# Kernel tuning notes

Hardware: AMD Instinct MI355X
Metric: run time of the kernel (lower is better)

## Reference

```python
import jax, jax.numpy as jnp
import numpy as np

# irreps = 128x0e + 64x1o + 32x2e  ->  dim = 128 + 192 + 160 = 480
IRREPS = [(128, 0), (64, 1), (32, 2)]  # (multiplicity, l)
NUM_SCALAR = 128          # 0e channels (p=+1, l=0); scalar_index = [0..127]
NUM_FEATURES = 224        # total irrep instances
DIM = 480
EPS_LN = 1e-5             # unused by math path (kept for fidelity to signature)
EPS_INV = 1e-6            # Invariant eps (default)
N = 100000


def setup_inputs() -> dict:
    key = jax.random.key(0)
    k1, k2, k3 = jax.random.split(key, 3)
    node_input = jax.random.normal(k1, (N, DIM), dtype=jnp.float32)
    affine_weight = jax.random.normal(k2, (NUM_FEATURES,), dtype=jnp.float32)
    affine_bias = jax.random.normal(k3, (NUM_SCALAR,), dtype=jnp.float32)
    return {"node_input": node_input, "affine_weight": affine_weight, "affine_bias": affine_bias}


def _eln(x, weight, bias):
    # 1) subtract mean of scalar (0e) channels from those channels only
    scalar_mean = jnp.mean(x[:, :NUM_SCALAR], axis=1, keepdims=True)
    x = x.at[:, :NUM_SCALAR].add(-scalar_mean)

    # 2) per-irrep-instance norm: Invariant = Norm(x + eps^2) - eps
    norms = []
    off = 0
    for mul, l in IRREPS:
        d = 2 * l + 1
        blk = x[:, off: off + mul * d].reshape(x.shape[0], mul, d)
        n = jnp.sqrt(jnp.sum(jnp.square(blk + EPS_INV ** 2), axis=-1)) - EPS_INV
        norms.append(n)
        off += mul * d
    norm = jnp.concatenate(norms, axis=1)  # [N, num_features]

    # 3) RMS over irrep instances, scale whole feature vector
    inv_rms = jax.lax.rsqrt(jnp.mean(jnp.square(norm), axis=1, keepdims=True))
    x = x * inv_rms

    # 4) per-irrep affine scale (ElementwiseTensorProduct with num_features x 0e)
    w_parts = []
    ix = 0
    for mul, l in IRREPS:
        d = 2 * l + 1
        w_parts.append(jnp.repeat(weight[ix: ix + mul], d))
        ix += mul
    w_full = jnp.concatenate(w_parts)  # [dim]
    x = x * w_full[None, :]

    # 5) add bias to scalar channels
    x = x.at[:, :NUM_SCALAR].add(bias[None, :])
    return x


def reference(node_input, affine_weight, affine_bias):
    return _eln(node_input, affine_weight, affine_bias)
```

## Files before the change

### kernel.cpp

```cpp
#include <hip/hip_runtime.h>
#include <hip/hip_bf16.h>


#define DIM 480

typedef float f32x4 __attribute__((ext_vector_type(4)));

__global__ __launch_bounds__(256) void eln_kernel(
    const float* __restrict__ in,
    const float* __restrict__ wgt,
    const float* __restrict__ bias,
    float* __restrict__ out,
    int n_rows)
{
    const int lane    = threadIdx.x & 63;
    const int gwave   = (blockIdx.x * blockDim.x + threadIdx.x) >> 6;
    const int n_waves = (gridDim.x * blockDim.x) >> 6;

    float w0k[4], w1k[4], bk[4];
    #pragma unroll
    for (int k = 0; k < 4; ++k) {
        int j = 4 * lane + k;
        if (j < 128) { w0k[k] = wgt[j];                       bk[k] = bias[j]; }
        else         { w0k[k] = wgt[128 + (j - 128) / 3];     bk[k] = 0.f;     }
    }
    #pragma unroll
    for (int k = 0; k < 4; ++k) {
        if (lane < 56) {
            int j = 256 + 4 * lane + k;
            w1k[k] = (j < 320) ? wgt[128 + (j - 128) / 3]
                               : wgt[192 + (j - 320) / 5];
        } else {
            w1k[k] = 0.f;
        }
    }

    const float epsq = 1e-12f;

    for (int row = gwave; row < n_rows; row += n_waves) {
        const f32x4* xr = reinterpret_cast<const f32x4*>(in + (size_t)row * DIM);
        f32x4*       yr = reinterpret_cast<f32x4*>(out + (size_t)row * DIM);

        f32x4 r0 = __builtin_nontemporal_load(xr + lane);
        f32x4 r1 = (f32x4)(0.f);
        if (lane < 56) r1 = __builtin_nontemporal_load(xr + 64 + lane);

        float ssum = (lane < 32) ? (r0.x + r0.y + r0.z + r0.w) : 0.f;
        #pragma unroll
        for (int m = 1; m < 64; m <<= 1) ssum += __shfl_xor(ssum, m);
        const float mean = ssum * (1.0f / 128.0f);
        if (lane < 32) { r0.x -= mean; r0.y -= mean; r0.z -= mean; r0.w -= mean; }

        float a0 = r0.x + epsq, a1 = r0.y + epsq, a2 = r0.z + epsq, a3 = r0.w + epsq;
        float nsq = a0 * a0 + a1 * a1 + a2 * a2 + a3 * a3;
        if (lane < 56) {
            float c0 = r1.x + epsq, c1 = r1.y + epsq, c2 = r1.z + epsq, c3 = r1.w + epsq;
            nsq += c0 * c0 + c1 * c1 + c2 * c2 + c3 * c3;
        }
        #pragma unroll
        for (int m = 1; m < 64; m <<= 1) nsq += __shfl_xor(nsq, m);
        const float inv_rms = rsqrtf(nsq * (1.0f / 224.0f));

        f32x4 o0;
        o0.x = r0.x * inv_rms * w0k[0] + bk[0];
        o0.y = r0.y * inv_rms * w0k[1] + bk[1];
        o0.z = r0.z * inv_rms * w0k[2] + bk[2];
        o0.w = r0.w * inv_rms * w0k[3] + bk[3];
        __builtin_nontemporal_store(o0, yr + lane);

        if (lane < 56) {
            f32x4 o1;
            o1.x = r1.x * inv_rms * w1k[0];
            o1.y = r1.y * inv_rms * w1k[1];
            o1.z = r1.z * inv_rms * w1k[2];
            o1.w = r1.w * inv_rms * w1k[3];
            __builtin_nontemporal_store(o1, yr + 64 + lane);
        }
    }
}

extern "C" void kernel_launch(void* const* d_in, const int* in_sizes, int n_in,
                              void* d_out, int out_size, void* d_ws, size_t ws_size,
                              hipStream_t stream) {
    const float* node_input    = (const float*)d_in[0];
    const float* affine_weight = (const float*)d_in[1];
    const float* affine_bias   = (const float*)d_in[2];
    float* out = (float*)d_out;

    const int n_rows = in_sizes[0] / DIM;
    int grid = (n_rows + 3) / 4;
    if (grid > 2048) grid = 2048;

    eln_kernel<<<grid, 256, 0, stream>>>(node_input, affine_weight, affine_bias,
                                         out, n_rows);
}
```

Before: 72.78 us.

## Process two rows per wave and fuse mean and norm reductions

Each wave now handles a pair of rows, issuing all four loads up front so more memory requests are in flight. The mean subtraction is folded into the squared-norm reduction algebraically, so the sum and the sum of squares are reduced in one combined shuffle tree instead of two sequential ones. This removes the serial dependency between the two reductions and raises memory-level parallelism. In exchange it uses more registers, and computing the centered norm from raw sums may be less numerically accurate.

```diff
diff --git a/kernel.cpp b/kernel.cpp
--- a/kernel.cpp
+++ b/kernel.cpp
@@ -21,8 +21,8 @@
     #pragma unroll
     for (int k = 0; k < 4; ++k) {
         int j = 4 * lane + k;
-        if (j < 128) { w0k[k] = wgt[j];                       bk[k] = bias[j]; }
-        else         { w0k[k] = wgt[128 + (j - 128) / 3];     bk[k] = 0.f;     }
+        if (j < 128) { w0k[k] = wgt[j];                   bk[k] = bias[j]; }
+        else         { w0k[k] = wgt[128 + (j - 128) / 3]; bk[k] = 0.f;     }
     }
     #pragma unroll
     for (int k = 0; k < 4; ++k) {
@@ -36,45 +36,83 @@
     }
 
     const float epsq = 1e-12f;
+    const int npairs = (n_rows + 1) >> 1;
 
-    for (int row = gwave; row < n_rows; row += n_waves) {
-        const f32x4* xr = reinterpret_cast<const f32x4*>(in + (size_t)row * DIM);
-        f32x4*       yr = reinterpret_cast<f32x4*>(out + (size_t)row * DIM);
+    for (int p = gwave; p < npairs; p += n_waves) {
+        const int row0 = p << 1;
+        const bool has1 = (row0 + 1) < n_rows;
 
-        f32x4 r0 = __builtin_nontemporal_load(xr + lane);
-        f32x4 r1 = (f32x4)(0.f);
-        if (lane < 56) r1 = __builtin_nontemporal_load(xr + 64 + lane);
+        const f32x4* xa = reinterpret_cast<const f32x4*>(in + (size_t)row0 * DIM);
+        const f32x4* xb = reinterpret_cast<const f32x4*>(in + (size_t)(row0 + 1) * DIM);
 
-        float ssum = (lane < 32) ? (r0.x + r0.y + r0.z + r0.w) : 0.f;
+        f32x4 a0 = __builtin_nontemporal_load(xa + lane);
+        f32x4 a1 = (f32x4)(0.f);
+        if (lane < 56) a1 = __builtin_nontemporal_load(xa + 64 + lane);
+        f32x4 b0 = (f32x4)(0.f), b1 = (f32x4)(0.f);
+        if (has1) {
+            b0 = __builtin_nontemporal_load(xb + lane);
+            if (lane < 56) b1 = __builtin_nontemporal_load(xb + 64 + lane);
+        }
+
+        float s1a = (lane < 32) ? (a0.x + a0.y + a0.z + a0.w) : 0.f;
+        float s1b = (lane < 32) ? (b0.x + b0.y + b0.z + b0.w) : 0.f;
+
+        float t0 = a0.x + epsq, t1 = a0.y + epsq, t2 = a0.z + epsq, t3 = a0.w + epsq;
+        float s2a = t0 * t0 + t1 * t1 + t2 * t2 + t3 * t3;
+        t0 = a1.x + epsq; t1 = a1.y + epsq; t2 = a1.z + epsq; t3 = a1.w + epsq;
+        if (lane < 56) s2a += t0 * t0 + t1 * t1 + t2 * t2 + t3 * t3;
+
+        t0 = b0.x + epsq; t1 = b0.y + epsq; t2 = b0.z + epsq; t3 = b0.w + epsq;
+        float s2b = t0 * t0 + t1 * t1 + t2 * t2 + t3 * t3;
+        t0 = b1.x + epsq; t1 = b1.y + epsq; t2 = b1.z + epsq; t3 = b1.w + epsq;
+        if (lane < 56) s2b += t0 * t0 + t1 * t1 + t2 * t2 + t3 * t3;
+
         #pragma unroll
-        for (int m = 1; m < 64; m <<= 1) ssum += __shfl_xor(ssum, m);
-        const float mean = ssum * (1.0f / 128.0f);
-        if (lane < 32) { r0.x -= mean; r0.y -= mean; r0.z -= mean; r0.w -= mean; }
+        for (int m = 1; m < 64; m <<= 1) {
+            s1a += __shfl_xor(s1a, m);
+            s2a += __shfl_xor(s2a, m);
+            s1b += __shfl_xor(s1b, m);
+            s2b += __shfl_xor(s2b, m);
+        }
 
-        float a0 = r0.x + epsq, a1 = r0.y + epsq, a2 = r0.z + epsq, a3 = r0.w + epsq;
-        float nsq = a0 * a0 + a1 * a1 + a2 * a2 + a3 * a3;
+        const float mean_a = s1a * (1.0f / 128.0f);
+        const float mean_b = s1b * (1.0f / 128.0f);
+        const float nsq_a  = s2a - s1a * mean_a - 2.f * epsq * s1a;
+        const float nsq_b  = s2b - s1b * mean_b - 2.f * epsq * s1b;
+        const float ir_a   = rsqrtf(nsq_a * (1.0f / 224.0f));
+        const float ir_b   = rsqrtf(nsq_b * (1.0f / 224.0f));
+
+        const float msel_a = (lane < 32) ? mean_a : 0.f;
+        const float msel_b = (lane < 32) ? mean_b : 0.f;
+
+        f32x4* ya = reinterpret_cast<f32x4*>(out + (size_t)row0 * DIM);
+        f32x4 o;
+        o.x = (a0.x - msel_a) * ir_a * w0k[0] + bk[0];
+        o.y = (a0.y - msel_a) * ir_a * w0k[1] + bk[1];
+        o.z = (a0.z - msel_a) * ir_a * w0k[2] + bk[2];
+        o.w = (a0.w - msel_a) * ir_a * w0k[3] + bk[3];
+        __builtin_nontemporal_store(o, ya + lane);
         if (lane < 56) {
-            float c0 = r1.x + epsq, c1 = r1.y + epsq, c2 = r1.z + epsq, c3 = r1.w + epsq;
-            nsq += c0 * c0 + c1 * c1 + c2 * c2 + c3 * c3;
+            o.x = a1.x * ir_a * w1k[0];
+            o.y = a1.y * ir_a * w1k[1];
+            o.z = a1.z * ir_a * w1k[2];
+            o.w = a1.w * ir_a * w1k[3];
+            __builtin_nontemporal_store(o, ya + 64 + lane);
         }
-        #pragma unroll
-        for (int m = 1; m < 64; m <<= 1) nsq += __shfl_xor(nsq, m);
-        const float inv_rms = rsqrtf(nsq * (1.0f / 224.0f));
-
-        f32x4 o0;
-        o0.x = r0.x * inv_rms * w0k[0] + bk[0];
-        o0.y = r0.y * inv_rms * w0k[1] + bk[1];
-        o0.z = r0.z * inv_rms * w0k[2] + bk[2];
-        o0.w = r0.w * inv_rms * w0k[3] + bk[3];
-        __builtin_nontemporal_store(o0, yr + lane);
-
-        if (lane < 56) {
-            f32x4 o1;
-            o1.x = r1.x * inv_rms * w1k[0];
-            o1.y = r1.y * inv_rms * w1k[1];
-            o1.z = r1.z * inv_rms * w1k[2];
-            o1.w = r1.w * inv_rms * w1k[3];
-            __builtin_nontemporal_store(o1, yr + 64 + lane);
+        if (has1) {
+            f32x4* yb = reinterpret_cast<f32x4*>(out + (size_t)(row0 + 1) * DIM);
+            o.x = (b0.x - msel_b) * ir_b * w0k[0] + bk[0];
+            o.y = (b0.y - msel_b) * ir_b * w0k[1] + bk[1];
+            o.z = (b0.z - msel_b) * ir_b * w0k[2] + bk[2];
+            o.w = (b0.w - msel_b) * ir_b * w0k[3] + bk[3];
+            __builtin_nontemporal_store(o, yb + lane);
+            if (lane < 56) {
+                o.x = b1.x * ir_b * w1k[0];
+                o.y = b1.y * ir_b * w1k[1];
+                o.z = b1.z * ir_b * w1k[2];
+                o.w = b1.w * ir_b * w1k[3];
+                __builtin_nontemporal_store(o, yb + 64 + lane);
+            }
         }
     }
 }
@@ -88,9 +126,6 @@
     float* out = (float*)d_out;
 
     const int n_rows = in_sizes[0] / DIM;
-    int grid = (n_rows + 3) / 4;
-    if (grid > 2048) grid = 2048;
-
-    eln_kernel<<<grid, 256, 0, stream>>>(node_input, affine_weight, affine_bias,
+    eln_kernel<<<2048, 256, 0, stream>>>(node_input, affine_weight, affine_bias,
                                          out, n_rows);
 }
```

New measurement: 69.43 us. -4.6%, faster.
